# Performance work log

Measured on AMD Instinct MI355X. Metric: run time of the kernel, lower is better.

The kernel has to match this reference:

```python
import jax, jax.numpy as jnp
import numpy as np

LN_EPS = 1e-5


def setup_inputs() -> dict:
    key = jax.random.key(0)
    ks = jax.random.split(key, 6)
    N, E, D = 100000, 600000, 128
    x = jax.random.normal(ks[0], (N, D), dtype=jnp.float32)
    edge_index = jax.random.randint(ks[1], (2, E), 0, N, dtype=jnp.int64)
    dropout_mask = jax.random.uniform(ks[2], (N, D), dtype=jnp.float32)
    ln_gamma = jnp.ones((D,), dtype=jnp.float32)
    ln_beta = jnp.zeros((D,), dtype=jnp.float32)
    W_l = jax.random.normal(ks[3], (D, D), dtype=jnp.float32) / np.sqrt(D)
    b_l = jnp.zeros((D,), dtype=jnp.float32)
    W_r = jax.random.normal(ks[4], (D, D), dtype=jnp.float32) / np.sqrt(D)
    return {"x": x, "edge_index": edge_index, "dropout_mask": dropout_mask,
            "ln_gamma": ln_gamma, "ln_beta": ln_beta,
            "W_l": W_l, "b_l": b_l, "W_r": W_r}


def reference(x, edge_index, dropout_mask, ln_gamma, ln_beta, W_l, b_l, W_r):
    N = x.shape[0]
    # LayerNorm (elementwise affine) -> ReLU -> dropout mask
    mu = jnp.mean(x, axis=-1, keepdims=True)
    var = jnp.mean(jnp.square(x - mu), axis=-1, keepdims=True)
    h = (x - mu) * jax.lax.rsqrt(var + LN_EPS) * ln_gamma + ln_beta
    h = jax.nn.relu(h) * dropout_mask  # [N, D]
    # SAGEConv with mean aggregation: messages flow src -> dst
    src, dst = edge_index[0], edge_index[1]
    agg = jax.ops.segment_sum(h[src], dst, num_segments=N)  # [N, D]
    cnt = jax.ops.segment_sum(jnp.ones_like(dst, dtype=h.dtype), dst,
                              num_segments=N)
    mean_agg = agg / jnp.maximum(cnt, 1.0)[:, None]
    # out = lin_l(mean_agg) + lin_r(h); PyG stores weights as [out, in]
    return mean_agg @ W_l.T + b_l + h @ W_r.T
```

## Files before the change

### kernel.cpp

```cpp
#include <hip/hip_runtime.h>

#define LN_EPS 1e-5f
#define D 128
#define SCAN_CHUNK 1024
#define LDSA_STRIDE 264

typedef __attribute__((ext_vector_type(4))) float f32x4;
typedef __attribute__((ext_vector_type(8))) short bf16x8;

static __device__ __forceinline__ ushort f2bf(float f) {
    union { float f; unsigned u; } a; a.f = f;
    unsigned r = a.u + 0x7FFF + ((a.u >> 16) & 1);
    return (ushort)(r >> 16);
}
static __device__ __forceinline__ float bf2f(ushort u) {
    union { unsigned u; float f; } a; a.u = ((unsigned)u) << 16;
    return a.f;
}

__global__ void ln_pack_hist(const float* __restrict__ x,
                             const float* __restrict__ mask,
                             const float* __restrict__ gamma,
                             const float* __restrict__ beta,
                             ushort* __restrict__ hbf,
                             const float* __restrict__ Wl,
                             const float* __restrict__ Wr,
                             ushort* __restrict__ Bfrag,
                             const int* __restrict__ ei,
                             int* __restrict__ hist,
                             int N, int E, int lnBlocks, int packBlocks) {
    int bid = (int)blockIdx.x;
    int tid = (int)threadIdx.x;

    if (bid >= lnBlocks + packBlocks) {
        int base = ((bid - lnBlocks - packBlocks) * 256 + tid) * 4;
        const int* dst = ei + E;
        if (base + 3 < E) {
            int4 d = *(const int4*)(dst + base);
            atomicAdd(&hist[d.x], 1);
            atomicAdd(&hist[d.y], 1);
            atomicAdd(&hist[d.z], 1);
            atomicAdd(&hist[d.w], 1);
        } else {
            for (int i = base; i < E && i < base + 4; i++)
                atomicAdd(&hist[dst[i]], 1);
        }
        return;
    }
    if (bid >= lnBlocks) {
        int t = (bid - lnBlocks) * 256 + tid;
        int i    = t & 7;
        int lane = (t >> 3) & 63;
        int jb   = (t >> 9) & 7;
        int ks   = t >> 12;
        int k = ks * 32 + (lane >> 4) * 8 + i;
        int j = jb * 16 + (lane & 15);
        float v = (k < D) ? Wl[j * D + k] : Wr[j * D + (k - D)];
        Bfrag[t] = f2bf(v);
        return;
    }

    int lane = tid & 63;
    int wid  = bid * 4 + (tid >> 6);
    int g2   = lane >> 4;
    int sl   = lane & 15;
    int nodeA = wid * 8 + g2;
    int nodeB = nodeA + 4;
    if (nodeA >= N) return;
    int nB = (nodeB < N) ? nodeB : nodeA;

    const float* xa = x + (size_t)nodeA * D + sl * 8;
    const float* xb = x + (size_t)nB * D + sl * 8;
    const float* ma = mask + (size_t)nodeA * D + sl * 8;
    const float* mb = mask + (size_t)nB * D + sl * 8;
    f32x4 va0 = *(const f32x4*)xa;
    f32x4 va1 = *(const f32x4*)(xa + 4);
    f32x4 vb0 = *(const f32x4*)xb;
    f32x4 vb1 = *(const f32x4*)(xb + 4);
    f32x4 ma0 = *(const f32x4*)ma;
    f32x4 ma1 = *(const f32x4*)(ma + 4);
    f32x4 mb0 = *(const f32x4*)mb;
    f32x4 mb1 = *(const f32x4*)(mb + 4);

    float sA  = (va0.x + va0.y) + (va0.z + va0.w) + (va1.x + va1.y) + (va1.z + va1.w);
    float ssA = (va0.x * va0.x + va0.y * va0.y) + (va0.z * va0.z + va0.w * va0.w)
              + (va1.x * va1.x + va1.y * va1.y) + (va1.z * va1.z + va1.w * va1.w);
    float sB  = (vb0.x + vb0.y) + (vb0.z + vb0.w) + (vb1.x + vb1.y) + (vb1.z + vb1.w);
    float ssB = (vb0.x * vb0.x + vb0.y * vb0.y) + (vb0.z * vb0.z + vb0.w * vb0.w)
              + (vb1.x * vb1.x + vb1.y * vb1.y) + (vb1.z * vb1.z + vb1.w * vb1.w);
#pragma unroll
    for (int off = 8; off > 0; off >>= 1) {
        sA  += __shfl_xor(sA, off);
        ssA += __shfl_xor(ssA, off);
        sB  += __shfl_xor(sB, off);
        ssB += __shfl_xor(ssB, off);
    }
    float muA = sA * (1.0f / D);
    float vrA = ssA * (1.0f / D) - muA * muA;
    float rsA = rsqrtf(vrA + LN_EPS);
    float muB = sB * (1.0f / D);
    float vrB = ssB * (1.0f / D) - muB * muB;
    float rsB = rsqrtf(vrB + LN_EPS);

    f32x4 g0 = *(const f32x4*)(gamma + sl * 8);
    f32x4 g1 = *(const f32x4*)(gamma + sl * 8 + 4);
    f32x4 b0 = *(const f32x4*)(beta + sl * 8);
    f32x4 b1 = *(const f32x4*)(beta + sl * 8 + 4);

    bf16x8 oA;
    oA[0] = (short)f2bf(fmaxf((va0.x - muA) * rsA * g0.x + b0.x, 0.0f) * ma0.x);
    oA[1] = (short)f2bf(fmaxf((va0.y - muA) * rsA * g0.y + b0.y, 0.0f) * ma0.y);
    oA[2] = (short)f2bf(fmaxf((va0.z - muA) * rsA * g0.z + b0.z, 0.0f) * ma0.z);
    oA[3] = (short)f2bf(fmaxf((va0.w - muA) * rsA * g0.w + b0.w, 0.0f) * ma0.w);
    oA[4] = (short)f2bf(fmaxf((va1.x - muA) * rsA * g1.x + b1.x, 0.0f) * ma1.x);
    oA[5] = (short)f2bf(fmaxf((va1.y - muA) * rsA * g1.y + b1.y, 0.0f) * ma1.y);
    oA[6] = (short)f2bf(fmaxf((va1.z - muA) * rsA * g1.z + b1.z, 0.0f) * ma1.z);
    oA[7] = (short)f2bf(fmaxf((va1.w - muA) * rsA * g1.w + b1.w, 0.0f) * ma1.w);
    *(bf16x8*)(hbf + (size_t)nodeA * D + sl * 8) = oA;

    if (nodeB < N) {
        bf16x8 oB;
        oB[0] = (short)f2bf(fmaxf((vb0.x - muB) * rsB * g0.x + b0.x, 0.0f) * mb0.x);
        oB[1] = (short)f2bf(fmaxf((vb0.y - muB) * rsB * g0.y + b0.y, 0.0f) * mb0.y);
        oB[2] = (short)f2bf(fmaxf((vb0.z - muB) * rsB * g0.z + b0.z, 0.0f) * mb0.z);
        oB[3] = (short)f2bf(fmaxf((vb0.w - muB) * rsB * g0.w + b0.w, 0.0f) * mb0.w);
        oB[4] = (short)f2bf(fmaxf((vb1.x - muB) * rsB * g1.x + b1.x, 0.0f) * mb1.x);
        oB[5] = (short)f2bf(fmaxf((vb1.y - muB) * rsB * g1.y + b1.y, 0.0f) * mb1.y);
        oB[6] = (short)f2bf(fmaxf((vb1.z - muB) * rsB * g1.z + b1.z, 0.0f) * mb1.z);
        oB[7] = (short)f2bf(fmaxf((vb1.w - muB) * rsB * g1.w + b1.w, 0.0f) * mb1.w);
        *(bf16x8*)(hbf + (size_t)nodeB * D + sl * 8) = oB;
    }
}

__global__ void scan_all(const int* __restrict__ hist, int* __restrict__ offs,
                         int* __restrict__ cursor, int* __restrict__ csums, int N) {
    __shared__ int lds[256];
    __shared__ int base_s;
    int base = blockIdx.x * SCAN_CHUNK;
    int t = threadIdx.x;
    int idx0 = base + t * 4;
    int v[4];
#pragma unroll
    for (int i = 0; i < 4; i++) {
        int idx = idx0 + i;
        v[i] = (idx < N) ? hist[idx] : 0;
    }
    lds[t] = v[0] + v[1] + v[2] + v[3];
    __syncthreads();
    for (int off = 1; off < 256; off <<= 1) {
        int add = (t >= off) ? lds[t - off] : 0;
        __syncthreads();
        lds[t] += add;
        __syncthreads();
    }
    int run = (t == 0) ? 0 : lds[t - 1];
    if (t == 255)
        __hip_atomic_store(&csums[blockIdx.x], lds[255] | 0x40000000,
                           __ATOMIC_RELEASE, __HIP_MEMORY_SCOPE_AGENT);
    if (t < 64) {
        int acc = 0;
        for (int c = t; c < (int)blockIdx.x; c += 64) {
            int w;
            do {
                w = __hip_atomic_load(&csums[c], __ATOMIC_ACQUIRE,
                                      __HIP_MEMORY_SCOPE_AGENT);
            } while (!(w & 0x40000000));
            acc += w & 0x3FFFFFFF;
        }
#pragma unroll
        for (int off = 32; off > 0; off >>= 1) acc += __shfl_xor(acc, off);
        if (t == 0) base_s = acc;
    }
    __syncthreads();
    run += base_s;
#pragma unroll
    for (int i = 0; i < 4; i++) {
        int idx = idx0 + i;
        if (idx < N) {
            offs[idx] = run;
            cursor[idx] = run;
        }
        run += v[i];
    }
}

__global__ void sort_edges(const int* __restrict__ ei, int* __restrict__ cursor,
                           int* __restrict__ sorted_src, int E) {
    int base = (blockIdx.x * blockDim.x + threadIdx.x) * 4;
    if (base >= E) return;
    if (base + 3 < E) {
        int4 d = *(const int4*)(ei + E + base);
        int4 s = *(const int4*)(ei + base);
        int p0 = atomicAdd(&cursor[d.x], 1);
        int p1 = atomicAdd(&cursor[d.y], 1);
        int p2 = atomicAdd(&cursor[d.z], 1);
        int p3 = atomicAdd(&cursor[d.w], 1);
        sorted_src[p0] = s.x;
        sorted_src[p1] = s.y;
        sorted_src[p2] = s.z;
        sorted_src[p3] = s.w;
    } else {
        for (int e = base; e < E; e++) {
            int pos = atomicAdd(&cursor[ei[E + e]], 1);
            sorted_src[pos] = ei[e];
        }
    }
}

__global__ void __launch_bounds__(256, 4)
agg_gemm(float* __restrict__ out,
         const ushort* __restrict__ hbf,
         const int* __restrict__ sorted_src,
         const int* __restrict__ offs,
         const int* __restrict__ hist,
         const ushort* __restrict__ Bfrag,
         const float* __restrict__ bl,
         int N, int E) {
    __shared__ ushort Alds[64 * LDSA_STRIDE];
    int tid  = threadIdx.x;
    int wave = tid >> 6;
    int lane = tid & 63;
    int n0 = blockIdx.x * 64;

#pragma unroll
    for (int it = 0; it < 4; it++) {
        int chunk = tid + 256 * it;
        int row = chunk >> 4;
        int c8  = chunk & 15;
        int node = n0 + row;
        bf16x8 vh = (bf16x8){0,0,0,0,0,0,0,0};
        if (node < N) vh = *(const bf16x8*)(hbf + (size_t)node * D + c8 * 8);
        *(bf16x8*)&Alds[row * LDSA_STRIDE + 128 + c8 * 8] = vh;
    }

    int g  = lane >> 4;
    int sl = lane & 15;
    int row0 = wave * 16 + g;
    int start[4], deg[4], dm1[4];
#pragma unroll
    for (int p = 0; p < 4; p++) {
        int node = n0 + row0 + p * 4;
        start[p] = 0; deg[p] = 0;
        if (node < N) { start[p] = offs[node]; deg[p] = hist[node]; }
        dm1[p] = deg[p] - 1; if (dm1[p] < 0) dm1[p] = 0;
    }
    float acc[4][8];
#pragma unroll
    for (int p = 0; p < 4; p++)
#pragma unroll
        for (int q = 0; q < 8; q++) acc[p][q] = 0.0f;

    int dmax = max(max(deg[0], deg[1]), max(deg[2], deg[3]));
    int Em = E - 1;
    int ia[4], ib[4];
#pragma unroll
    for (int p = 0; p < 4; p++) {
        int pa = start[p];                         if (pa > Em) pa = Em;
        int j1 = (1 < dm1[p]) ? 1 : dm1[p];
        int pb = start[p] + j1;                    if (pb > Em) pb = Em;
        ia[p] = sorted_src[pa];
        ib[p] = sorted_src[pb];
    }
    for (int j = 0; j < dmax; j += 2) {
        int ca[4], cb[4];
#pragma unroll
        for (int p = 0; p < 4; p++) { ca[p] = ia[p]; cb[p] = ib[p]; }
#pragma unroll
        for (int p = 0; p < 4; p++) {
            int j2 = (j + 2 < dm1[p]) ? j + 2 : dm1[p];
            int j3 = (j + 3 < dm1[p]) ? j + 3 : dm1[p];
            int pa = start[p] + j2; if (pa > Em) pa = Em;
            int pb = start[p] + j3; if (pb > Em) pb = Em;
            ia[p] = sorted_src[pa];
            ib[p] = sorted_src[pb];
        }
#pragma unroll
        for (int p = 0; p < 4; p++) {
            bf16x8 v = *(const bf16x8*)(hbf + (size_t)ca[p] * D + sl * 8);
            float m = (j < deg[p]) ? 1.0f : 0.0f;
#pragma unroll
            for (int q = 0; q < 8; q++) acc[p][q] += bf2f((ushort)v[q]) * m;
        }
#pragma unroll
        for (int p = 0; p < 4; p++) {
            bf16x8 v = *(const bf16x8*)(hbf + (size_t)cb[p] * D + sl * 8);
            float m = (j + 1 < deg[p]) ? 1.0f : 0.0f;
#pragma unroll
            for (int q = 0; q < 8; q++) acc[p][q] += bf2f((ushort)v[q]) * m;
        }
    }
#pragma unroll
    for (int p = 0; p < 4; p++) {
        float inv = 1.0f / fmaxf((float)deg[p], 1.0f);
        bf16x8 o;
#pragma unroll
        for (int q = 0; q < 8; q++) o[q] = (short)f2bf(acc[p][q] * inv);
        *(bf16x8*)&Alds[(row0 + p * 4) * LDSA_STRIDE + sl * 8] = o;
    }
    __syncthreads();

    bf16x8 breg[8][2];
#pragma unroll
    for (int ks = 0; ks < 8; ks++)
#pragma unroll
        for (int jj = 0; jj < 2; jj++) {
            int jb = wave * 2 + jj;
            breg[ks][jj] = *(const bf16x8*)(Bfrag + (size_t)((ks * 8 + jb) * 64 + lane) * 8);
        }

    f32x4 acc2[4][2];
#pragma unroll
    for (int nb = 0; nb < 4; nb++)
#pragma unroll
        for (int jj = 0; jj < 2; jj++)
            acc2[nb][jj] = (f32x4){0.f, 0.f, 0.f, 0.f};

    int arow = lane & 15;
    int akoff = (lane >> 4) * 8;
#pragma unroll
    for (int ks = 0; ks < 8; ks++) {
#pragma unroll
        for (int nb = 0; nb < 4; nb++) {
            bf16x8 a = *(const bf16x8*)&Alds[(nb * 16 + arow) * LDSA_STRIDE + ks * 32 + akoff];
            acc2[nb][0] = __builtin_amdgcn_mfma_f32_16x16x32_bf16(a, breg[ks][0], acc2[nb][0], 0, 0, 0);
            acc2[nb][1] = __builtin_amdgcn_mfma_f32_16x16x32_bf16(a, breg[ks][1], acc2[nb][1], 0, 0, 0);
        }
    }

    __syncthreads();
    float* fl = (float*)Alds;
    float bias0 = bl[wave * 32 + (lane & 15)];
    float bias1 = bl[wave * 32 + 16 + (lane & 15)];
    int rbase = (lane >> 4) * 4;
    int c0 = wave * 32 + (lane & 15);
#pragma unroll
    for (int nb = 0; nb < 4; nb++) {
#pragma unroll
        for (int r = 0; r < 4; r++) {
            int row = nb * 16 + rbase + r;
            fl[row * 128 + c0]      = acc2[nb][0][r] + bias0;
            fl[row * 128 + c0 + 16] = acc2[nb][1][r] + bias1;
        }
    }
    __syncthreads();
#pragma unroll
    for (int it = 0; it < 8; it++) {
        int c = tid + it * 256;
        int row = c >> 5;
        int q   = c & 31;
        if (n0 + row < N)
            *(f32x4*)(out + (size_t)(n0 + row) * D + q * 4) =
                *(const f32x4*)&fl[row * 128 + q * 4];
    }
}

extern "C" void kernel_launch(void* const* d_in, const int* in_sizes, int n_in,
                              void* d_out, int out_size, void* d_ws, size_t ws_size,
                              hipStream_t stream) {
    const float* x     = (const float*)d_in[0];
    const int*   ei    = (const int*)  d_in[1];
    const float* mask  = (const float*)d_in[2];
    const float* gamma = (const float*)d_in[3];
    const float* beta  = (const float*)d_in[4];
    const float* Wl    = (const float*)d_in[5];
    const float* bl    = (const float*)d_in[6];
    const float* Wr    = (const float*)d_in[7];
    float* out = (float*)d_out;

    int N = in_sizes[0] / D;
    int E = in_sizes[1] / 2;
    int chunks = (N + SCAN_CHUNK - 1) / SCAN_CHUNK;

    ushort* hbf   = (ushort*)d_ws;
    ushort* Bfrag = hbf + (size_t)N * D;
    int* hist   = (int*)(Bfrag + 32768);
    int* csums  = hist + N;
    int* offs   = csums + 128;
    int* cursor = offs + N;
    int* ssrc   = cursor + N;

    int lnBlocks   = (N + 31) / 32;
    int packBlocks = 128;
    int histBlocks = (E + 1023) / 1024;

    hipMemsetAsync(hist, 0, (size_t)(N + 128) * sizeof(int), stream);
    ln_pack_hist<<<lnBlocks + packBlocks + histBlocks, 256, 0, stream>>>(
        x, mask, gamma, beta, hbf, Wl, Wr, Bfrag, ei, hist, N, E,
        lnBlocks, packBlocks);
    scan_all<<<chunks, 256, 0, stream>>>(hist, offs, cursor, csums, N);
    sort_edges<<<(E / 4 + 255) / 256, 256, 0, stream>>>(ei, cursor, ssrc, E);
    agg_gemm<<<(N + 63) / 64, 256, 0, stream>>>(out, hbf, ssrc, offs, hist,
                                                Bfrag, bl, N, E);
}
```

Before: 255.0 us.

## Shrink aggregation tiles, deepen gather prefetch, and grid-stride the LayerNorm blocks

The agg_gemm kernel now handles 32 rows per block instead of 64, with launch bounds raised to 8 blocks per SM. Each lane now handles 2 nodes and prefetches 4 neighbour indices at a time instead of 2, to keep more gathers in flight and raise occupancy. The LayerNorm part of the first kernel now runs on a fixed 1536-block grid and loops over nodes with a grid stride, which cuts block count and lets the hist blocks start sooner. The costs are more blocks for the GEMM, each reloading the B fragments for fewer rows, and possible register pressure under the tighter launch bound.

```diff
diff --git a/kernel.cpp b/kernel.cpp
--- a/kernel.cpp
+++ b/kernel.cpp
@@ -4,6 +4,8 @@
 #define D 128
 #define SCAN_CHUNK 1024
 #define LDSA_STRIDE 264
+#define AGG_ROWS 32
+#define LNB 1536
 
 typedef __attribute__((ext_vector_type(4))) float f32x4;
 typedef __attribute__((ext_vector_type(8))) short bf16x8;
@@ -28,12 +30,12 @@
                              ushort* __restrict__ Bfrag,
                              const int* __restrict__ ei,
                              int* __restrict__ hist,
-                             int N, int E, int lnBlocks, int packBlocks) {
+                             int N, int E) {
     int bid = (int)blockIdx.x;
     int tid = (int)threadIdx.x;
 
-    if (bid >= lnBlocks + packBlocks) {
-        int base = ((bid - lnBlocks - packBlocks) * 256 + tid) * 4;
+    if (bid >= LNB + 128) {
+        int base = ((bid - LNB - 128) * 256 + tid) * 4;
         const int* dst = ei + E;
         if (base + 3 < E) {
             int4 d = *(const int4*)(dst + base);
@@ -47,8 +49,8 @@
         }
         return;
     }
-    if (bid >= lnBlocks) {
-        int t = (bid - lnBlocks) * 256 + tid;
+    if (bid >= LNB) {
+        int t = (bid - LNB) * 256 + tid;
         int i    = t & 7;
         int lane = (t >> 3) & 63;
         int jb   = (t >> 9) & 7;
@@ -62,73 +64,77 @@
 
     int lane = tid & 63;
     int wid  = bid * 4 + (tid >> 6);
+    int nw   = LNB * 4;
     int g2   = lane >> 4;
     int sl   = lane & 15;
-    int nodeA = wid * 8 + g2;
-    int nodeB = nodeA + 4;
-    if (nodeA >= N) return;
-    int nB = (nodeB < N) ? nodeB : nodeA;
-
-    const float* xa = x + (size_t)nodeA * D + sl * 8;
-    const float* xb = x + (size_t)nB * D + sl * 8;
-    const float* ma = mask + (size_t)nodeA * D + sl * 8;
-    const float* mb = mask + (size_t)nB * D + sl * 8;
-    f32x4 va0 = *(const f32x4*)xa;
-    f32x4 va1 = *(const f32x4*)(xa + 4);
-    f32x4 vb0 = *(const f32x4*)xb;
-    f32x4 vb1 = *(const f32x4*)(xb + 4);
-    f32x4 ma0 = *(const f32x4*)ma;
-    f32x4 ma1 = *(const f32x4*)(ma + 4);
-    f32x4 mb0 = *(const f32x4*)mb;
-    f32x4 mb1 = *(const f32x4*)(mb + 4);
-
-    float sA  = (va0.x + va0.y) + (va0.z + va0.w) + (va1.x + va1.y) + (va1.z + va1.w);
-    float ssA = (va0.x * va0.x + va0.y * va0.y) + (va0.z * va0.z + va0.w * va0.w)
-              + (va1.x * va1.x + va1.y * va1.y) + (va1.z * va1.z + va1.w * va1.w);
-    float sB  = (vb0.x + vb0.y) + (vb0.z + vb0.w) + (vb1.x + vb1.y) + (vb1.z + vb1.w);
-    float ssB = (vb0.x * vb0.x + vb0.y * vb0.y) + (vb0.z * vb0.z + vb0.w * vb0.w)
-              + (vb1.x * vb1.x + vb1.y * vb1.y) + (vb1.z * vb1.z + vb1.w * vb1.w);
-#pragma unroll
-    for (int off = 8; off > 0; off >>= 1) {
-        sA  += __shfl_xor(sA, off);
-        ssA += __shfl_xor(ssA, off);
-        sB  += __shfl_xor(sB, off);
-        ssB += __shfl_xor(ssB, off);
-    }
-    float muA = sA * (1.0f / D);
-    float vrA = ssA * (1.0f / D) - muA * muA;
-    float rsA = rsqrtf(vrA + LN_EPS);
-    float muB = sB * (1.0f / D);
-    float vrB = ssB * (1.0f / D) - muB * muB;
-    float rsB = rsqrtf(vrB + LN_EPS);
 
     f32x4 g0 = *(const f32x4*)(gamma + sl * 8);
     f32x4 g1 = *(const f32x4*)(gamma + sl * 8 + 4);
     f32x4 b0 = *(const f32x4*)(beta + sl * 8);
     f32x4 b1 = *(const f32x4*)(beta + sl * 8 + 4);
 
-    bf16x8 oA;
-    oA[0] = (short)f2bf(fmaxf((va0.x - muA) * rsA * g0.x + b0.x, 0.0f) * ma0.x);
-    oA[1] = (short)f2bf(fmaxf((va0.y - muA) * rsA * g0.y + b0.y, 0.0f) * ma0.y);
-    oA[2] = (short)f2bf(fmaxf((va0.z - muA) * rsA * g0.z + b0.z, 0.0f) * ma0.z);
-    oA[3] = (short)f2bf(fmaxf((va0.w - muA) * rsA * g0.w + b0.w, 0.0f) * ma0.w);
-    oA[4] = (short)f2bf(fmaxf((va1.x - muA) * rsA * g1.x + b1.x, 0.0f) * ma1.x);
-    oA[5] = (short)f2bf(fmaxf((va1.y - muA) * rsA * g1.y + b1.y, 0.0f) * ma1.y);
-    oA[6] = (short)f2bf(fmaxf((va1.z - muA) * rsA * g1.z + b1.z, 0.0f) * ma1.z);
-    oA[7] = (short)f2bf(fmaxf((va1.w - muA) * rsA * g1.w + b1.w, 0.0f) * ma1.w);
-    *(bf16x8*)(hbf + (size_t)nodeA * D + sl * 8) = oA;
-
-    if (nodeB < N) {
-        bf16x8 oB;
-        oB[0] = (short)f2bf(fmaxf((vb0.x - muB) * rsB * g0.x + b0.x, 0.0f) * mb0.x);
-        oB[1] = (short)f2bf(fmaxf((vb0.y - muB) * rsB * g0.y + b0.y, 0.0f) * mb0.y);
-        oB[2] = (short)f2bf(fmaxf((vb0.z - muB) * rsB * g0.z + b0.z, 0.0f) * mb0.z);
-        oB[3] = (short)f2bf(fmaxf((vb0.w - muB) * rsB * g0.w + b0.w, 0.0f) * mb0.w);
-        oB[4] = (short)f2bf(fmaxf((vb1.x - muB) * rsB * g1.x + b1.x, 0.0f) * mb1.x);
-        oB[5] = (short)f2bf(fmaxf((vb1.y - muB) * rsB * g1.y + b1.y, 0.0f) * mb1.y);
-        oB[6] = (short)f2bf(fmaxf((vb1.z - muB) * rsB * g1.z + b1.z, 0.0f) * mb1.z);
-        oB[7] = (short)f2bf(fmaxf((vb1.w - muB) * rsB * g1.w + b1.w, 0.0f) * mb1.w);
-        *(bf16x8*)(hbf + (size_t)nodeB * D + sl * 8) = oB;
+    for (int np = wid; np * 8 < N; np += nw) {
+        int nodeA = np * 8 + g2;
+        int nodeB = nodeA + 4;
+        if (nodeA >= N) continue;
+        int nB = (nodeB < N) ? nodeB : nodeA;
+
+        const float* xa = x + (size_t)nodeA * D + sl * 8;
+        const float* xb = x + (size_t)nB * D + sl * 8;
+        const float* ma = mask + (size_t)nodeA * D + sl * 8;
+        const float* mb = mask + (size_t)nB * D + sl * 8;
+        f32x4 va0 = *(const f32x4*)xa;
+        f32x4 va1 = *(const f32x4*)(xa + 4);
+        f32x4 vb0 = *(const f32x4*)xb;
+        f32x4 vb1 = *(const f32x4*)(xb + 4);
+        f32x4 ma0 = *(const f32x4*)ma;
+        f32x4 ma1 = *(const f32x4*)(ma + 4);
+        f32x4 mb0 = *(const f32x4*)mb;
+        f32x4 mb1 = *(const f32x4*)(mb + 4);
+
+        float sA  = (va0.x + va0.y) + (va0.z + va0.w) + (va1.x + va1.y) + (va1.z + va1.w);
+        float ssA = (va0.x * va0.x + va0.y * va0.y) + (va0.z * va0.z + va0.w * va0.w)
+                  + (va1.x * va1.x + va1.y * va1.y) + (va1.z * va1.z + va1.w * va1.w);
+        float sB  = (vb0.x + vb0.y) + (vb0.z + vb0.w) + (vb1.x + vb1.y) + (vb1.z + vb1.w);
+        float ssB = (vb0.x * vb0.x + vb0.y * vb0.y) + (vb0.z * vb0.z + vb0.w * vb0.w)
+                  + (vb1.x * vb1.x + vb1.y * vb1.y) + (vb1.z * vb1.z + vb1.w * vb1.w);
+#pragma unroll
+        for (int off = 8; off > 0; off >>= 1) {
+            sA  += __shfl_xor(sA, off);
+            ssA += __shfl_xor(ssA, off);
+            sB  += __shfl_xor(sB, off);
+            ssB += __shfl_xor(ssB, off);
+        }
+        float muA = sA * (1.0f / D);
+        float vrA = ssA * (1.0f / D) - muA * muA;
+        float rsA = rsqrtf(vrA + LN_EPS);
+        float muB = sB * (1.0f / D);
+        float vrB = ssB * (1.0f / D) - muB * muB;
+        float rsB = rsqrtf(vrB + LN_EPS);
+
+        bf16x8 oA;
+        oA[0] = (short)f2bf(fmaxf((va0.x - muA) * rsA * g0.x + b0.x, 0.0f) * ma0.x);
+        oA[1] = (short)f2bf(fmaxf((va0.y - muA) * rsA * g0.y + b0.y, 0.0f) * ma0.y);
+        oA[2] = (short)f2bf(fmaxf((va0.z - muA) * rsA * g0.z + b0.z, 0.0f) * ma0.z);
+        oA[3] = (short)f2bf(fmaxf((va0.w - muA) * rsA * g0.w + b0.w, 0.0f) * ma0.w);
+        oA[4] = (short)f2bf(fmaxf((va1.x - muA) * rsA * g1.x + b1.x, 0.0f) * ma1.x);
+        oA[5] = (short)f2bf(fmaxf((va1.y - muA) * rsA * g1.y + b1.y, 0.0f) * ma1.y);
+        oA[6] = (short)f2bf(fmaxf((va1.z - muA) * rsA * g1.z + b1.z, 0.0f) * ma1.z);
+        oA[7] = (short)f2bf(fmaxf((va1.w - muA) * rsA * g1.w + b1.w, 0.0f) * ma1.w);
+        *(bf16x8*)(hbf + (size_t)nodeA * D + sl * 8) = oA;
+
+        if (nodeB < N) {
+            bf16x8 oB;
+            oB[0] = (short)f2bf(fmaxf((vb0.x - muB) * rsB * g0.x + b0.x, 0.0f) * mb0.x);
+            oB[1] = (short)f2bf(fmaxf((vb0.y - muB) * rsB * g0.y + b0.y, 0.0f) * mb0.y);
+            oB[2] = (short)f2bf(fmaxf((vb0.z - muB) * rsB * g0.z + b0.z, 0.0f) * mb0.z);
+            oB[3] = (short)f2bf(fmaxf((vb0.w - muB) * rsB * g0.w + b0.w, 0.0f) * mb0.w);
+            oB[4] = (short)f2bf(fmaxf((vb1.x - muB) * rsB * g1.x + b1.x, 0.0f) * mb1.x);
+            oB[5] = (short)f2bf(fmaxf((vb1.y - muB) * rsB * g1.y + b1.y, 0.0f) * mb1.y);
+            oB[6] = (short)f2bf(fmaxf((vb1.z - muB) * rsB * g1.z + b1.z, 0.0f) * mb1.z);
+            oB[7] = (short)f2bf(fmaxf((vb1.w - muB) * rsB * g1.w + b1.w, 0.0f) * mb1.w);
+            *(bf16x8*)(hbf + (size_t)nodeB * D + sl * 8) = oB;
+        }
     }
 }
 
@@ -207,7 +213,7 @@
     }
 }
 
-__global__ void __launch_bounds__(256, 4)
+__global__ void __launch_bounds__(256, 8)
 agg_gemm(float* __restrict__ out,
          const ushort* __restrict__ hbf,
          const int* __restrict__ sorted_src,
@@ -216,14 +222,14 @@
          const ushort* __restrict__ Bfrag,
          const float* __restrict__ bl,
          int N, int E) {
-    __shared__ ushort Alds[64 * LDSA_STRIDE];
+    __shared__ ushort Alds[AGG_ROWS * LDSA_STRIDE];
     int tid  = threadIdx.x;
     int wave = tid >> 6;
     int lane = tid & 63;
-    int n0 = blockIdx.x * 64;
-
-#pragma unroll
-    for (int it = 0; it < 4; it++) {
+    int n0 = blockIdx.x * AGG_ROWS;
+
+#pragma unroll
+    for (int it = 0; it < 2; it++) {
         int chunk = tid + 256 * it;
         int row = chunk >> 4;
         int c8  = chunk & 15;
@@ -235,62 +241,59 @@
 
     int g  = lane >> 4;
     int sl = lane & 15;
-    int row0 = wave * 16 + g;
-    int start[4], deg[4], dm1[4];
-#pragma unroll
-    for (int p = 0; p < 4; p++) {
+    int row0 = wave * 8 + g;
+    int start[2], deg[2], dm1[2];
+#pragma unroll
+    for (int p = 0; p < 2; p++) {
         int node = n0 + row0 + p * 4;
         start[p] = 0; deg[p] = 0;
         if (node < N) { start[p] = offs[node]; deg[p] = hist[node]; }
         dm1[p] = deg[p] - 1; if (dm1[p] < 0) dm1[p] = 0;
     }
-    float acc[4][8];
-#pragma unroll
-    for (int p = 0; p < 4; p++)
+    float acc[2][8];
+#pragma unroll
+    for (int p = 0; p < 2; p++)
 #pragma unroll
         for (int q = 0; q < 8; q++) acc[p][q] = 0.0f;
 
-    int dmax = max(max(deg[0], deg[1]), max(deg[2], deg[3]));
+    int dmax = max(deg[0], deg[1]);
     int Em = E - 1;
-    int ia[4], ib[4];
-#pragma unroll
-    for (int p = 0; p < 4; p++) {
-        int pa = start[p];                         if (pa > Em) pa = Em;
-        int j1 = (1 < dm1[p]) ? 1 : dm1[p];
-        int pb = start[p] + j1;                    if (pb > Em) pb = Em;
-        ia[p] = sorted_src[pa];
-        ib[p] = sorted_src[pb];
-    }
-    for (int j = 0; j < dmax; j += 2) {
-        int ca[4], cb[4];
-#pragma unroll
-        for (int p = 0; p < 4; p++) { ca[p] = ia[p]; cb[p] = ib[p]; }
-#pragma unroll
-        for (int p = 0; p < 4; p++) {
-            int j2 = (j + 2 < dm1[p]) ? j + 2 : dm1[p];
-            int j3 = (j + 3 < dm1[p]) ? j + 3 : dm1[p];
-            int pa = start[p] + j2; if (pa > Em) pa = Em;
-            int pb = start[p] + j3; if (pb > Em) pb = Em;
-            ia[p] = sorted_src[pa];
-            ib[p] = sorted_src[pb];
-        }
-#pragma unroll
-        for (int p = 0; p < 4; p++) {
-            bf16x8 v = *(const bf16x8*)(hbf + (size_t)ca[p] * D + sl * 8);
-            float m = (j < deg[p]) ? 1.0f : 0.0f;
-#pragma unroll
-            for (int q = 0; q < 8; q++) acc[p][q] += bf2f((ushort)v[q]) * m;
-        }
-#pragma unroll
-        for (int p = 0; p < 4; p++) {
-            bf16x8 v = *(const bf16x8*)(hbf + (size_t)cb[p] * D + sl * 8);
-            float m = (j + 1 < deg[p]) ? 1.0f : 0.0f;
-#pragma unroll
-            for (int q = 0; q < 8; q++) acc[p][q] += bf2f((ushort)v[q]) * m;
-        }
-    }
-#pragma unroll
-    for (int p = 0; p < 4; p++) {
+    int idx[4][2];
+#pragma unroll
+    for (int k = 0; k < 4; k++)
+#pragma unroll
+        for (int p = 0; p < 2; p++) {
+            int jc = (k < dm1[p]) ? k : dm1[p];
+            int pos = start[p] + jc; if (pos > Em) pos = Em;
+            idx[k][p] = sorted_src[pos];
+        }
+    for (int j = 0; j < dmax; j += 4) {
+        int cur[4][2];
+#pragma unroll
+        for (int k = 0; k < 4; k++)
+#pragma unroll
+            for (int p = 0; p < 2; p++) cur[k][p] = idx[k][p];
+#pragma unroll
+        for (int k = 0; k < 4; k++)
+#pragma unroll
+            for (int p = 0; p < 2; p++) {
+                int jn = j + 4 + k; jn = (jn < dm1[p]) ? jn : dm1[p];
+                int pos = start[p] + jn; if (pos > Em) pos = Em;
+                idx[k][p] = sorted_src[pos];
+            }
+#pragma unroll
+        for (int k = 0; k < 4; k++) {
+#pragma unroll
+            for (int p = 0; p < 2; p++) {
+                bf16x8 v = *(const bf16x8*)(hbf + (size_t)cur[k][p] * D + sl * 8);
+                float m = (j + k < deg[p]) ? 1.0f : 0.0f;
+#pragma unroll
+                for (int q = 0; q < 8; q++) acc[p][q] += bf2f((ushort)v[q]) * m;
+            }
+        }
+    }
+#pragma unroll
+    for (int p = 0; p < 2; p++) {
         float inv = 1.0f / fmaxf((float)deg[p], 1.0f);
         bf16x8 o;
 #pragma unroll
@@ -308,9 +311,9 @@
             breg[ks][jj] = *(const bf16x8*)(Bfrag + (size_t)((ks * 8 + jb) * 64 + lane) * 8);
         }
 
-    f32x4 acc2[4][2];
-#pragma unroll
-    for (int nb = 0; nb < 4; nb++)
+    f32x4 acc2[2][2];
+#pragma unroll
+    for (int nb = 0; nb < 2; nb++)
 #pragma unroll
         for (int jj = 0; jj < 2; jj++)
             acc2[nb][jj] = (f32x4){0.f, 0.f, 0.f, 0.f};
@@ -320,7 +323,7 @@
 #pragma unroll
     for (int ks = 0; ks < 8; ks++) {
 #pragma unroll
-        for (int nb = 0; nb < 4; nb++) {
+        for (int nb = 0; nb < 2; nb++) {
             bf16x8 a = *(const bf16x8*)&Alds[(nb * 16 + arow) * LDSA_STRIDE + ks * 32 + akoff];
             acc2[nb][0] = __builtin_amdgcn_mfma_f32_16x16x32_bf16(a, breg[ks][0], acc2[nb][0], 0, 0, 0);
             acc2[nb][1] = __builtin_amdgcn_mfma_f32_16x16x32_bf16(a, breg[ks][1], acc2[nb][1], 0, 0, 0);
@@ -334,7 +337,7 @@
     int rbase = (lane >> 4) * 4;
     int c0 = wave * 32 + (lane & 15);
 #pragma unroll
-    for (int nb = 0; nb < 4; nb++) {
+    for (int nb = 0; nb < 2; nb++) {
 #pragma unroll
         for (int r = 0; r < 4; r++) {
             int row = nb * 16 + rbase + r;
@@ -344,7 +347,7 @@
     }
     __syncthreads();
 #pragma unroll
-    for (int it = 0; it < 8; it++) {
+    for (int it = 0; it < 4; it++) {
         int c = tid + it * 256;
         int row = c >> 5;
         int q   = c & 31;
@@ -379,16 +382,13 @@
     int* cursor = offs + N;
     int* ssrc   = cursor + N;
 
-    int lnBlocks   = (N + 31) / 32;
-    int packBlocks = 128;
     int histBlocks = (E + 1023) / 1024;
 
     hipMemsetAsync(hist, 0, (size_t)(N + 128) * sizeof(int), stream);
-    ln_pack_hist<<<lnBlocks + packBlocks + histBlocks, 256, 0, stream>>>(
-        x, mask, gamma, beta, hbf, Wl, Wr, Bfrag, ei, hist, N, E,
-        lnBlocks, packBlocks);
+    ln_pack_hist<<<LNB + 128 + histBlocks, 256, 0, stream>>>(
+        x, mask, gamma, beta, hbf, Wl, Wr, Bfrag, ei, hist, N, E);
     scan_all<<<chunks, 256, 0, stream>>>(hist, offs, cursor, csums, N);
     sort_edges<<<(E / 4 + 255) / 256, 256, 0, stream>>>(ei, cursor, ssrc, E);
-    agg_gemm<<<(N + 63) / 64, 256, 0, stream>>>(out, hbf, ssrc, offs, hist,
-                                                Bfrag, bl, N, E);
-}
+    agg_gemm<<<(N + AGG_ROWS - 1) / AGG_ROWS, 256, 0, stream>>>(
+        out, hbf, ssrc, offs, hist, Bfrag, bl, N, E);
+}
```

Result: slower. 291.3 us (+14.2%).
